# Performance work log

Hardware: AMD Instinct MI355X
Metric: run time of the kernel (lower is better)

The kernel has to match this reference:

```python
import jax, jax.numpy as jnp
from jax import lax
import numpy as np

T, B, D, H = 512, 256, 128, 256
SHIFT = 0.0


def setup_inputs() -> dict:
    key = jax.random.key(0)
    ks = jax.random.split(key, 11)
    s_in = 1.0 / np.sqrt(D + H)
    s_cl = 1.0 / np.sqrt(H)
    return {
        "inputs": jax.random.normal(ks[0], (T, B, D), dtype=jnp.float32),
        "Wf": jax.random.normal(ks[1], (H, D + H), dtype=jnp.float32) * s_in,
        "bf": jax.random.normal(ks[2], (H,), dtype=jnp.float32) * s_in,
        "Wi": jax.random.normal(ks[3], (H, D + H), dtype=jnp.float32) * s_in,
        "bi": jax.random.normal(ks[4], (H,), dtype=jnp.float32) * s_in,
        "Wg": jax.random.normal(ks[5], (H, D + H), dtype=jnp.float32) * s_in,
        "bg": jax.random.normal(ks[6], (H,), dtype=jnp.float32) * s_in,
        "Wo": jax.random.normal(ks[7], (H, D + H), dtype=jnp.float32) * s_in,
        "bo": jax.random.normal(ks[8], (H,), dtype=jnp.float32) * s_in,
        "Wc": jax.random.normal(ks[9], (1, H), dtype=jnp.float32) * s_cl,
        "bc": jax.random.normal(ks[10], (1,), dtype=jnp.float32) * s_cl,
    }


def reference(inputs, Wf, bf, Wi, bi, Wg, bg, Wo, bo, Wc, bc):
    # Fuse the four gate linears into one GEMM per step: [4H, D+H]
    W = jnp.concatenate([Wf, Wi, Wg, Wo], axis=0)
    b = jnp.concatenate([bf, bi, bg, bo], axis=0)
    h = W.shape[0] // 4
    batch = inputs.shape[1]

    def step(carry, x):
        hx, cx = carry
        combined = jnp.concatenate([x, hx], axis=1)      # [B, D+H]
        z = combined @ W.T + b                            # [B, 4H]
        f = jax.nn.sigmoid(z[:, 0 * h:1 * h])
        i = jax.nn.sigmoid(z[:, 1 * h:2 * h])
        g = jnp.tanh(z[:, 2 * h:3 * h])
        o = jax.nn.sigmoid(z[:, 3 * h:4 * h])
        cx = f * cx + i * g
        hx = o * jnp.tanh(cx)
        return (hx, cx), hx

    h0 = jnp.zeros((batch, h), dtype=inputs.dtype)
    c0 = jnp.zeros((batch, h), dtype=inputs.dtype)
    (hx, cx), hs = lax.scan(step, (h0, c0), inputs)       # hs: [T, B, H]

    logits = hs @ Wc.T + bc                               # [T, B, 1]
    probs = jax.nn.sigmoid(logits + SHIFT)
    return (jnp.concatenate([probs, 1.0 - probs], axis=-1), hx, cx)
```

## Files before the change

kernel.cpp:

```cpp
#include <hip/hip_runtime.h>
#include <hip/hip_bf16.h>
#include <hip/hip_cooperative_groups.h>

namespace cg = cooperative_groups;


#define T_STEPS 512
#define BATCH   256
#define DIN     128
#define HID     256
#define KDIM    384
#define LDK     392
#define GRIDN   256
#define NPOLL   96

typedef __attribute__((ext_vector_type(8))) short short8;
typedef __attribute__((ext_vector_type(4))) short short4v;
typedef __attribute__((ext_vector_type(4))) float f32x4;

__device__ unsigned boot_percxd[8];
__device__ unsigned boot_claimed[8];

__device__ __forceinline__ unsigned short f2bf(float f) {
    unsigned u = __float_as_uint(f);
    unsigned r = (u + 0x7FFFu + ((u >> 16) & 1u)) >> 16;
    return (unsigned short)r;
}
__device__ __forceinline__ float bf2f(unsigned short s) {
    return __uint_as_float(((unsigned)s) << 16);
}
__device__ __forceinline__ float sigmoid_f(float x) {
    return 1.f / (1.f + __expf(-x));
}
__device__ __forceinline__ float tanh_f(float x) {
    float e = __expf(2.f * x);
    return 1.f - 2.f / (e + 1.f);
}
__device__ __forceinline__ void poll_load_sc0(const unsigned int* p, uint4& a,
                                              uint4& b, uint4& c, uint4& d) {
    asm volatile(
        "global_load_dwordx4 %0, %4, off sc0\n\t"
        "global_load_dwordx4 %1, %4, off offset:16 sc0\n\t"
        "global_load_dwordx4 %2, %4, off offset:32 sc0\n\t"
        "global_load_dwordx4 %3, %4, off offset:48 sc0\n\t"
        "s_waitcnt vmcnt(0)"
        : "=&v"(a), "=&v"(b), "=&v"(c), "=&v"(d) : "v"(p) : "memory");
}
__device__ __forceinline__ void poll_load_sc1(const unsigned int* p, uint4& a,
                                              uint4& b, uint4& c, uint4& d) {
    asm volatile(
        "global_load_dwordx4 %0, %4, off sc1\n\t"
        "global_load_dwordx4 %1, %4, off offset:16 sc1\n\t"
        "global_load_dwordx4 %2, %4, off offset:32 sc1\n\t"
        "global_load_dwordx4 %3, %4, off offset:48 sc1\n\t"
        "s_waitcnt vmcnt(0)"
        : "=&v"(a), "=&v"(b), "=&v"(c), "=&v"(d) : "v"(p) : "memory");
}
__device__ __forceinline__ void store_plain_u32(unsigned int* p, unsigned int v) {
    asm volatile("global_store_dword %0, %1, off" :: "v"(p), "v"(v) : "memory");
}
__device__ __forceinline__ void store_sc1_u32(unsigned int* p, unsigned int v) {
    asm volatile("global_store_dword %0, %1, off sc1" :: "v"(p), "v"(v) : "memory");
}
__device__ __forceinline__ unsigned pack2bf(unsigned lo, unsigned hi) {
    return (hi & 0xFFFF0000u) | (lo >> 16);
}
__device__ __forceinline__ bool tags_ok(const uint4& a, const uint4& b,
                                        const uint4& c, const uint4& d,
                                        unsigned tag) {
    return ((a.x ^ tag) & 0xFFFFu) == 0 && ((a.y ^ tag) & 0xFFFFu) == 0 &&
           ((a.z ^ tag) & 0xFFFFu) == 0 && ((a.w ^ tag) & 0xFFFFu) == 0 &&
           ((b.x ^ tag) & 0xFFFFu) == 0 && ((b.y ^ tag) & 0xFFFFu) == 0 &&
           ((b.z ^ tag) & 0xFFFFu) == 0 && ((b.w ^ tag) & 0xFFFFu) == 0 &&
           ((c.x ^ tag) & 0xFFFFu) == 0 && ((c.y ^ tag) & 0xFFFFu) == 0 &&
           ((c.z ^ tag) & 0xFFFFu) == 0 && ((c.w ^ tag) & 0xFFFFu) == 0 &&
           ((d.x ^ tag) & 0xFFFFu) == 0 && ((d.y ^ tag) & 0xFFFFu) == 0 &&
           ((d.z ^ tag) & 0xFFFFu) == 0 && ((d.w ^ tag) & 0xFFFFu) == 0;
}

__global__ __launch_bounds__(256) void pack_w(
    const float* __restrict__ Wf, const float* __restrict__ Wi,
    const float* __restrict__ Wg, const float* __restrict__ Wo,
    unsigned short* __restrict__ Wp) {
    int idx = blockIdx.x * 256 + threadIdx.x;
    int n = idx / KDIM;
    int k = idx - n * KDIM;
    int g = n >> 8, j = n & 255;
    const float* s = (g == 0) ? Wf : (g == 1) ? Wi : (g == 2) ? Wg : Wo;
    Wp[idx] = f2bf(s[j * KDIM + k]);
}

__global__ __launch_bounds__(256) void pack_b(
    const float* __restrict__ bf, const float* __restrict__ bi,
    const float* __restrict__ bg, const float* __restrict__ bo,
    float* __restrict__ bp) {
    int n = blockIdx.x * 256 + threadIdx.x;
    int g = n >> 8, j = n & 255;
    const float* s = (g == 0) ? bf : (g == 1) ? bi : (g == 2) ? bg : bo;
    bp[n] = s[j];
}

__global__ __launch_bounds__(256) void init_k(unsigned int* __restrict__ hxp) {
    int tid = blockIdx.x * 256 + threadIdx.x;
    hxp[tid] = 0u;
    hxp[65536 + tid] = 0u;
    hxp[131072 + tid] = 0u;
    hxp[196608 + tid] = 0u;
    if (tid < 8) {
        boot_percxd[tid] = 0u;
        boot_claimed[tid] = 0u;
    }
}

__global__ __launch_bounds__(256, 1) void lstm_persist(
    const float* __restrict__ X,
    const unsigned short* __restrict__ W,
    const float* __restrict__ bias,
    unsigned int* __restrict__ hxp,
    unsigned short* __restrict__ hist,
    float* __restrict__ out) {
    __shared__ __align__(16) unsigned short W_s[64 * LDK];
    __shared__ __align__(16) unsigned short comb_s[16 * LDK];
    __shared__ __align__(16) float z_s[4 * 272];
    __shared__ int fastok_s;
    __shared__ int role_s;

    const int tid = threadIdx.x;

    if (tid == 0) {
        unsigned xcc = __builtin_amdgcn_s_getreg((31u << 11) | 20u) & 7u;
        unsigned slot = atomicAdd(&boot_percxd[xcc], 1u);
        int role = -1;
        if (slot < 32u) {
            role = (int)(xcc * 32u + slot);
            atomicOr(&boot_claimed[role >> 5], 1u << (role & 31));
        }
        role_s = role;
        fastok_s = 1;
    }
    __syncthreads();
    cg::this_grid().sync();
    if (role_s < 0) {
        if (tid == 0) {
            for (int r = 0; r < 256; ++r) {
                unsigned bit = 1u << (r & 31);
                if (!(atomicOr(&boot_claimed[r >> 5], bit) & bit)) {
                    role_s = r;
                    break;
                }
            }
        }
        __syncthreads();
    }
    const int role = role_s;
    const int bg = role >> 4, jg = role & 15;
    const int b0 = bg * 16, j0 = jg * 16;
    const int wave = tid >> 6, lane = tid & 63;
    const int l16 = lane & 15, quad = lane >> 4;
    const int bi = tid >> 4, jj = tid & 15;
    const int b = b0 + bi, j = j0 + jj;

#pragma unroll
    for (int c = 0; c < 12; ++c) {
        int q = c * 256 + tid;
        int row = q / 48, c8 = q - row * 48;
        int g = row >> 4, jr = row & 15;
        short8 v = *(const short8*)(W + ((g * 256 + j0 + jr) * KDIM + c8 * 8));
        *(short8*)(&W_s[row * LDK + c8 * 8]) = v;
    }
    const float bs0 = bias[0 * HID + j];
    const float bs1 = bias[1 * HID + j];
    const float bs2 = bias[2 * HID + j];
    const float bs3 = bias[3 * HID + j];

    float c_reg = 0.f;
    float h_final = 0.f;

    const unsigned short* arow = &comb_s[l16 * LDK + quad * 8];
    const unsigned short* brow = &W_s[(wave * 16 + l16) * LDK + quad * 8];
    const int hrow = tid >> 4, hc = tid & 15;
    const int xr0 = tid >> 5, xc4 = tid & 31, xr1 = (tid + 256) >> 5;

    const float* xb = X + b0 * DIN;
    float4 xv0 = *(const float4*)(xb + xr0 * DIN + xc4 * 4);
    float4 xv1 = *(const float4*)(xb + xr1 * DIN + xc4 * 4);

    __syncthreads();

    for (int k = 0; k < T_STEPS; ++k) {
        const unsigned tag = (unsigned)k;
        const unsigned int* fb =
            hxp + (k & 1) * 65536 + (b0 + hrow) * HID + hc * 16;
        const unsigned int* sb = fb + 131072;
        uint4 a, bq, cq, d;
        const int usefast = fastok_s;

        {
            short4v r;
            r.x = (short)f2bf(xv0.x); r.y = (short)f2bf(xv0.y);
            r.z = (short)f2bf(xv0.z); r.w = (short)f2bf(xv0.w);
            *(short4v*)(&comb_s[xr0 * LDK + xc4 * 4]) = r;
            r.x = (short)f2bf(xv1.x); r.y = (short)f2bf(xv1.y);
            r.z = (short)f2bf(xv1.z); r.w = (short)f2bf(xv1.w);
            *(short4v*)(&comb_s[xr1 * LDK + xc4 * 4]) = r;
        }

        if (usefast) {
            int tries = NPOLL;
            bool ok = false;
            for (;;) {
                poll_load_sc0(fb, a, bq, cq, d);
                if (tags_ok(a, bq, cq, d, tag)) { ok = true; break; }
                if (--tries == 0) break;
            }
            if (!ok) {
                fastok_s = 0;
                for (;;) {
                    poll_load_sc1(sb, a, bq, cq, d);
                    if (tags_ok(a, bq, cq, d, tag)) break;
                    __builtin_amdgcn_s_sleep(1);
                }
            }
        } else {
            for (;;) {
                poll_load_sc1(sb, a, bq, cq, d);
                if (tags_ok(a, bq, cq, d, tag)) break;
                __builtin_amdgcn_s_sleep(1);
            }
        }

        {
            uint4 p0, p1;
            p0.x = pack2bf(a.x, a.y);   p0.y = pack2bf(a.z, a.w);
            p0.z = pack2bf(bq.x, bq.y); p0.w = pack2bf(bq.z, bq.w);
            p1.x = pack2bf(cq.x, cq.y); p1.y = pack2bf(cq.z, cq.w);
            p1.z = pack2bf(d.x, d.y);   p1.w = pack2bf(d.z, d.w);
            *(uint4*)(&comb_s[hrow * LDK + DIN + hc * 16]) = p0;
            *(uint4*)(&comb_s[hrow * LDK + DIN + hc * 16 + 8]) = p1;
        }
        __syncthreads();

        f32x4 acc0 = {0.f, 0.f, 0.f, 0.f}, acc1 = {0.f, 0.f, 0.f, 0.f};
#pragma unroll
        for (int kt = 0; kt < 6; ++kt) {
            short8 a0 = *(const short8*)(arow + (2 * kt) * 32);
            short8 b0v = *(const short8*)(brow + (2 * kt) * 32);
            short8 a1 = *(const short8*)(arow + (2 * kt + 1) * 32);
            short8 b1v = *(const short8*)(brow + (2 * kt + 1) * 32);
            acc0 = __builtin_amdgcn_mfma_f32_16x16x32_bf16(a0, b0v, acc0, 0, 0, 0);
            acc1 = __builtin_amdgcn_mfma_f32_16x16x32_bf16(a1, b1v, acc1, 0, 0, 0);
        }
#pragma unroll
        for (int r = 0; r < 4; ++r)
            z_s[wave * 272 + (quad * 4 + r) * 17 + l16] = acc0[r] + acc1[r];
        __syncthreads();

        float zf = z_s[0 * 272 + bi * 17 + jj] + bs0;
        float zi = z_s[1 * 272 + bi * 17 + jj] + bs1;
        float zg = z_s[2 * 272 + bi * 17 + jj] + bs2;
        float zo = z_s[3 * 272 + bi * 17 + jj] + bs3;
        float fg = sigmoid_f(zf);
        float ig = sigmoid_f(zi);
        float gg = tanh_f(zg);
        float og = sigmoid_f(zo);
        c_reg = fg * c_reg + ig * gg;
        float hval = og * tanh_f(c_reg);
        unsigned short hb = f2bf(hval);
        unsigned int hword = ((unsigned)hb << 16) | (unsigned)(k + 1);
        unsigned int* fdst = hxp + ((k + 1) & 1) * 65536 + b * HID + j;
        store_plain_u32(fdst, hword);
        store_sc1_u32(fdst + 131072, hword);
        hist[(size_t)k * BATCH * HID + b * HID + j] = hb;
        if (k + 1 < T_STEPS) {
            const float* xn = X + (size_t)(k + 1) * BATCH * DIN + b0 * DIN;
            xv0 = *(const float4*)(xn + xr0 * DIN + xc4 * 4);
            xv1 = *(const float4*)(xn + xr1 * DIN + xc4 * 4);
        } else {
            h_final = hval;
        }
    }

    out[T_STEPS * BATCH * 2 + b * HID + j] = h_final;
    out[T_STEPS * BATCH * 2 + BATCH * HID + b * HID + j] = c_reg;
}

__global__ __launch_bounds__(256) void probs_k(
    const unsigned short* __restrict__ hist, const float* __restrict__ Wc,
    const float* __restrict__ bc, float* __restrict__ out) {
    const int wave = threadIdx.x >> 6, lane = threadIdx.x & 63;
    const size_t row = (size_t)blockIdx.x * 4 + wave;
    const unsigned short* h = hist + row * HID;
    short4v hv = *(const short4v*)(h + lane * 4);
    const float4 wv = *(const float4*)(Wc + lane * 4);
    float p = bf2f((unsigned short)hv.x) * wv.x + bf2f((unsigned short)hv.y) * wv.y +
              bf2f((unsigned short)hv.z) * wv.z + bf2f((unsigned short)hv.w) * wv.w;
#pragma unroll
    for (int off = 32; off >= 1; off >>= 1) p += __shfl_down(p, off);
    if (lane == 0) {
        float prob = 1.f / (1.f + __expf(-(p + bc[0])));
        out[row * 2]     = prob;
        out[row * 2 + 1] = 1.f - prob;
    }
}

extern "C" void kernel_launch(void* const* d_in, const int* in_sizes, int n_in,
                              void* d_out, int out_size, void* d_ws, size_t ws_size,
                              hipStream_t stream) {
    const float* X  = (const float*)d_in[0];
    const float* Wf = (const float*)d_in[1];
    const float* bfp= (const float*)d_in[2];
    const float* Wi = (const float*)d_in[3];
    const float* bip= (const float*)d_in[4];
    const float* Wg = (const float*)d_in[5];
    const float* bgp= (const float*)d_in[6];
    const float* Wo = (const float*)d_in[7];
    const float* bop= (const float*)d_in[8];
    const float* Wc = (const float*)d_in[9];
    const float* bc = (const float*)d_in[10];
    float* out = (float*)d_out;

    char* ws = (char*)d_ws;
    unsigned short* Wpack = (unsigned short*)(ws);
    float* bias = (float*)(ws + 786432);
    unsigned int* hxp = (unsigned int*)(ws + 790528);
    unsigned short* hist = (unsigned short*)(ws + 1839104);

    pack_w<<<1536, 256, 0, stream>>>(Wf, Wi, Wg, Wo, Wpack);
    pack_b<<<4, 256, 0, stream>>>(bfp, bip, bgp, bop, bias);
    init_k<<<256, 256, 0, stream>>>(hxp);

    void* kargs[6] = {(void*)&X, (void*)&Wpack, (void*)&bias,
                      (void*)&hxp, (void*)&hist, (void*)&out};
    (void)hipLaunchCooperativeKernel((const void*)lstm_persist, dim3(GRIDN),
                                     dim3(256), kargs, 0, stream);

    probs_k<<<32768, 256, 0, stream>>>(hist, Wc, bc, out);
}
```

Before: 1.203 ms.

## Add helper wave for slow-path publishing and history stores in persistent LSTM

Adds a fifth wavefront per block that picks up freshly computed h words from LDS and issues the sc1 slow-path global stores and the bf16 history writes. The compute waves no longer stall on those stores. The change also double-buffers the X prefetch two steps ahead and moves the next step's X conversion into the post-GEMM phase. The trade-off is a larger block, extra LDS polling and a padding array that forces one block per CU, plus the risk that the slow-path publication now lags by a wave handoff.

```diff
diff --git a/kernel.cpp b/kernel.cpp
--- a/kernel.cpp
+++ b/kernel.cpp
@@ -12,6 +12,8 @@
 #define KDIM    384
 #define LDK     392
 #define GRIDN   256
+#define BLOCKT  320
+#define NCOMP   256
 #define NPOLL   96
 
 typedef __attribute__((ext_vector_type(8))) short short8;
@@ -112,7 +114,7 @@
     }
 }
 
-__global__ __launch_bounds__(256, 1) void lstm_persist(
+__global__ __launch_bounds__(BLOCKT, 1) void lstm_persist(
     const float* __restrict__ X,
     const unsigned short* __restrict__ W,
     const float* __restrict__ bias,
@@ -122,6 +124,8 @@
     __shared__ __align__(16) unsigned short W_s[64 * LDK];
     __shared__ __align__(16) unsigned short comb_s[16 * LDK];
     __shared__ __align__(16) float z_s[4 * 272];
+    __shared__ __align__(16) unsigned hw_lds[NCOMP];
+    __shared__ char pad_s[32768];
     __shared__ int fastok_s;
     __shared__ int role_s;
 
@@ -153,6 +157,8 @@
         __syncthreads();
     }
     const int role = role_s;
+    if (role == -12345) pad_s[0] = 1;
+
     const int bg = role >> 4, jg = role & 15;
     const int b0 = bg * 16, j0 = jg * 16;
     const int wave = tid >> 6, lane = tid & 63;
@@ -160,18 +166,24 @@
     const int bi = tid >> 4, jj = tid & 15;
     const int b = b0 + bi, j = j0 + jj;
 
+    if (tid < NCOMP) {
 #pragma unroll
-    for (int c = 0; c < 12; ++c) {
-        int q = c * 256 + tid;
-        int row = q / 48, c8 = q - row * 48;
-        int g = row >> 4, jr = row & 15;
-        short8 v = *(const short8*)(W + ((g * 256 + j0 + jr) * KDIM + c8 * 8));
-        *(short8*)(&W_s[row * LDK + c8 * 8]) = v;
-    }
-    const float bs0 = bias[0 * HID + j];
-    const float bs1 = bias[1 * HID + j];
-    const float bs2 = bias[2 * HID + j];
-    const float bs3 = bias[3 * HID + j];
+        for (int c = 0; c < 12; ++c) {
+            int q = c * 256 + tid;
+            int row = q / 48, c8 = q - row * 48;
+            int g = row >> 4, jr = row & 15;
+            short8 v = *(const short8*)(W + ((g * 256 + j0 + jr) * KDIM + c8 * 8));
+            *(short8*)(&W_s[row * LDK + c8 * 8]) = v;
+        }
+        hw_lds[tid] = 0u;
+    }
+    float bs0 = 0.f, bs1 = 0.f, bs2 = 0.f, bs3 = 0.f;
+    if (tid < NCOMP) {
+        bs0 = bias[0 * HID + j];
+        bs1 = bias[1 * HID + j];
+        bs2 = bias[2 * HID + j];
+        bs3 = bias[3 * HID + j];
+    }
 
     float c_reg = 0.f;
     float h_final = 0.f;
@@ -181,55 +193,73 @@
     const int hrow = tid >> 4, hc = tid & 15;
     const int xr0 = tid >> 5, xc4 = tid & 31, xr1 = (tid + 256) >> 5;
 
-    const float* xb = X + b0 * DIN;
-    float4 xv0 = *(const float4*)(xb + xr0 * DIN + xc4 * 4);
-    float4 xv1 = *(const float4*)(xb + xr1 * DIN + xc4 * 4);
-
+    const int sv = tid - NCOMP;
+    const int t4 = sv * 4;
+    const int bs_b = b0 + (t4 >> 4), bs_j = j0 + (t4 & 15);
+
+    float4 xA0, xA1, xB0, xB1;
+    if (tid < NCOMP) {
+        const float* x0b = X + b0 * DIN;
+        float4 t0 = *(const float4*)(x0b + xr0 * DIN + xc4 * 4);
+        float4 t1 = *(const float4*)(x0b + xr1 * DIN + xc4 * 4);
+        short4v r;
+        r.x = (short)f2bf(t0.x); r.y = (short)f2bf(t0.y);
+        r.z = (short)f2bf(t0.z); r.w = (short)f2bf(t0.w);
+        *(short4v*)(&comb_s[xr0 * LDK + xc4 * 4]) = r;
+        r.x = (short)f2bf(t1.x); r.y = (short)f2bf(t1.y);
+        r.z = (short)f2bf(t1.z); r.w = (short)f2bf(t1.w);
+        *(short4v*)(&comb_s[xr1 * LDK + xc4 * 4]) = r;
+        const float* x1b = X + (size_t)1 * BATCH * DIN + b0 * DIN;
+        xB0 = *(const float4*)(x1b + xr0 * DIN + xc4 * 4);
+        xB1 = *(const float4*)(x1b + xr1 * DIN + xc4 * 4);
+    }
     __syncthreads();
 
     for (int k = 0; k < T_STEPS; ++k) {
-        const unsigned tag = (unsigned)k;
-        const unsigned int* fb =
-            hxp + (k & 1) * 65536 + (b0 + hrow) * HID + hc * 16;
-        const unsigned int* sb = fb + 131072;
-        uint4 a, bq, cq, d;
-        const int usefast = fastok_s;
-
-        {
-            short4v r;
-            r.x = (short)f2bf(xv0.x); r.y = (short)f2bf(xv0.y);
-            r.z = (short)f2bf(xv0.z); r.w = (short)f2bf(xv0.w);
-            *(short4v*)(&comb_s[xr0 * LDK + xc4 * 4]) = r;
-            r.x = (short)f2bf(xv1.x); r.y = (short)f2bf(xv1.y);
-            r.z = (short)f2bf(xv1.z); r.w = (short)f2bf(xv1.w);
-            *(short4v*)(&comb_s[xr1 * LDK + xc4 * 4]) = r;
-        }
-
-        if (usefast) {
-            int tries = NPOLL;
-            bool ok = false;
-            for (;;) {
-                poll_load_sc0(fb, a, bq, cq, d);
-                if (tags_ok(a, bq, cq, d, tag)) { ok = true; break; }
-                if (--tries == 0) break;
-            }
-            if (!ok) {
-                fastok_s = 0;
+        if (tid < NCOMP) {
+            const unsigned tag = (unsigned)k;
+            const unsigned int* fb =
+                hxp + (k & 1) * 65536 + (b0 + hrow) * HID + hc * 16;
+            const unsigned int* sb = fb + 131072;
+            uint4 a, bq, cq, d;
+            const int usefast = fastok_s;
+
+            if (usefast) {
+                int tries = NPOLL;
+                bool ok = false;
+                for (;;) {
+                    poll_load_sc0(fb, a, bq, cq, d);
+                    if (tags_ok(a, bq, cq, d, tag)) { ok = true; break; }
+                    if (--tries == 0) break;
+                }
+                if (!ok) {
+                    fastok_s = 0;
+                    for (;;) {
+                        poll_load_sc1(sb, a, bq, cq, d);
+                        if (tags_ok(a, bq, cq, d, tag)) break;
+                        __builtin_amdgcn_s_sleep(1);
+                    }
+                }
+            } else {
                 for (;;) {
                     poll_load_sc1(sb, a, bq, cq, d);
                     if (tags_ok(a, bq, cq, d, tag)) break;
                     __builtin_amdgcn_s_sleep(1);
                 }
             }
-        } else {
-            for (;;) {
-                poll_load_sc1(sb, a, bq, cq, d);
-                if (tags_ok(a, bq, cq, d, tag)) break;
-                __builtin_amdgcn_s_sleep(1);
-            }
-        }
-
-        {
+
+            if (k + 2 < T_STEPS) {
+                const float* xn = X + (size_t)(k + 2) * BATCH * DIN + b0 * DIN;
+                if (k & 1) {
+                    xB0 = *(const float4*)(xn + xr0 * DIN + xc4 * 4);
+                    xB1 = *(const float4*)(xn + xr1 * DIN + xc4 * 4);
+                } else {
+                    xA0 = *(const float4*)(xn + xr0 * DIN + xc4 * 4);
+                    xA1 = *(const float4*)(xn + xr1 * DIN + xc4 * 4);
+                }
+            }
+            __builtin_amdgcn_sched_barrier(0);
+
             uint4 p0, p1;
             p0.x = pack2bf(a.x, a.y);   p0.y = pack2bf(a.z, a.w);
             p0.z = pack2bf(bq.x, bq.y); p0.w = pack2bf(bq.z, bq.w);
@@ -237,51 +267,104 @@
             p1.z = pack2bf(d.x, d.y);   p1.w = pack2bf(d.z, d.w);
             *(uint4*)(&comb_s[hrow * LDK + DIN + hc * 16]) = p0;
             *(uint4*)(&comb_s[hrow * LDK + DIN + hc * 16 + 8]) = p1;
+        } else if (k > 0) {
+            volatile unsigned* hw = hw_lds;
+            unsigned w0, w1, w2, w3;
+            const unsigned tag = (unsigned)k;
+            for (;;) {
+                w0 = hw[t4]; w1 = hw[t4 + 1]; w2 = hw[t4 + 2]; w3 = hw[t4 + 3];
+                if (((w0 ^ tag) & 0xFFFFu) == 0 && ((w1 ^ tag) & 0xFFFFu) == 0 &&
+                    ((w2 ^ tag) & 0xFFFFu) == 0 && ((w3 ^ tag) & 0xFFFFu) == 0)
+                    break;
+            }
+            unsigned int* sd =
+                hxp + 131072 + (k & 1) * 65536 + bs_b * HID + bs_j;
+            store_sc1_u32(sd + 0, w0);
+            store_sc1_u32(sd + 1, w1);
+            store_sc1_u32(sd + 2, w2);
+            store_sc1_u32(sd + 3, w3);
+            uint2 hp;
+            hp.x = pack2bf(w0, w1);
+            hp.y = pack2bf(w2, w3);
+            *(uint2*)(&hist[(size_t)(k - 1) * BATCH * HID +
+                            (size_t)bs_b * HID + bs_j]) = hp;
+            asm volatile("s_waitcnt vmcnt(16)" ::: "memory");
         }
         __syncthreads();
 
-        f32x4 acc0 = {0.f, 0.f, 0.f, 0.f}, acc1 = {0.f, 0.f, 0.f, 0.f};
+        if (tid < NCOMP) {
+            f32x4 acc0 = {0.f, 0.f, 0.f, 0.f}, acc1 = {0.f, 0.f, 0.f, 0.f};
 #pragma unroll
-        for (int kt = 0; kt < 6; ++kt) {
-            short8 a0 = *(const short8*)(arow + (2 * kt) * 32);
-            short8 b0v = *(const short8*)(brow + (2 * kt) * 32);
-            short8 a1 = *(const short8*)(arow + (2 * kt + 1) * 32);
-            short8 b1v = *(const short8*)(brow + (2 * kt + 1) * 32);
-            acc0 = __builtin_amdgcn_mfma_f32_16x16x32_bf16(a0, b0v, acc0, 0, 0, 0);
-            acc1 = __builtin_amdgcn_mfma_f32_16x16x32_bf16(a1, b1v, acc1, 0, 0, 0);
-        }
+            for (int kt = 0; kt < 6; ++kt) {
+                short8 a0 = *(const short8*)(arow + (2 * kt) * 32);
+                short8 b0v = *(const short8*)(brow + (2 * kt) * 32);
+                short8 a1 = *(const short8*)(arow + (2 * kt + 1) * 32);
+                short8 b1v = *(const short8*)(brow + (2 * kt + 1) * 32);
+                acc0 = __builtin_amdgcn_mfma_f32_16x16x32_bf16(a0, b0v, acc0, 0, 0, 0);
+                acc1 = __builtin_amdgcn_mfma_f32_16x16x32_bf16(a1, b1v, acc1, 0, 0, 0);
+            }
 #pragma unroll
-        for (int r = 0; r < 4; ++r)
-            z_s[wave * 272 + (quad * 4 + r) * 17 + l16] = acc0[r] + acc1[r];
+            for (int r = 0; r < 4; ++r)
+                z_s[wave * 272 + (quad * 4 + r) * 17 + l16] = acc0[r] + acc1[r];
+        }
         __syncthreads();
 
-        float zf = z_s[0 * 272 + bi * 17 + jj] + bs0;
-        float zi = z_s[1 * 272 + bi * 17 + jj] + bs1;
-        float zg = z_s[2 * 272 + bi * 17 + jj] + bs2;
-        float zo = z_s[3 * 272 + bi * 17 + jj] + bs3;
-        float fg = sigmoid_f(zf);
-        float ig = sigmoid_f(zi);
-        float gg = tanh_f(zg);
-        float og = sigmoid_f(zo);
-        c_reg = fg * c_reg + ig * gg;
-        float hval = og * tanh_f(c_reg);
-        unsigned short hb = f2bf(hval);
-        unsigned int hword = ((unsigned)hb << 16) | (unsigned)(k + 1);
-        unsigned int* fdst = hxp + ((k + 1) & 1) * 65536 + b * HID + j;
-        store_plain_u32(fdst, hword);
-        store_sc1_u32(fdst + 131072, hword);
-        hist[(size_t)k * BATCH * HID + b * HID + j] = hb;
-        if (k + 1 < T_STEPS) {
-            const float* xn = X + (size_t)(k + 1) * BATCH * DIN + b0 * DIN;
-            xv0 = *(const float4*)(xn + xr0 * DIN + xc4 * 4);
-            xv1 = *(const float4*)(xn + xr1 * DIN + xc4 * 4);
-        } else {
-            h_final = hval;
-        }
-    }
-
-    out[T_STEPS * BATCH * 2 + b * HID + j] = h_final;
-    out[T_STEPS * BATCH * 2 + BATCH * HID + b * HID + j] = c_reg;
+        if (tid < NCOMP) {
+            if (k + 1 < T_STEPS) {
+                float4 s0 = ((k + 1) & 1) ? xB0 : xA0;
+                float4 s1 = ((k + 1) & 1) ? xB1 : xA1;
+                short4v r;
+                r.x = (short)f2bf(s0.x); r.y = (short)f2bf(s0.y);
+                r.z = (short)f2bf(s0.z); r.w = (short)f2bf(s0.w);
+                *(short4v*)(&comb_s[xr0 * LDK + xc4 * 4]) = r;
+                r.x = (short)f2bf(s1.x); r.y = (short)f2bf(s1.y);
+                r.z = (short)f2bf(s1.z); r.w = (short)f2bf(s1.w);
+                *(short4v*)(&comb_s[xr1 * LDK + xc4 * 4]) = r;
+            }
+            float zf = z_s[0 * 272 + bi * 17 + jj] + bs0;
+            float zi = z_s[1 * 272 + bi * 17 + jj] + bs1;
+            float zg = z_s[2 * 272 + bi * 17 + jj] + bs2;
+            float zo = z_s[3 * 272 + bi * 17 + jj] + bs3;
+            float fg = sigmoid_f(zf);
+            float ig = sigmoid_f(zi);
+            float gg = tanh_f(zg);
+            float og = sigmoid_f(zo);
+            c_reg = fg * c_reg + ig * gg;
+            float hval = og * tanh_f(c_reg);
+            unsigned short hb = f2bf(hval);
+            unsigned int hword = ((unsigned)hb << 16) | (unsigned)(k + 1);
+            unsigned int* fdst = hxp + ((k + 1) & 1) * 65536 + b * HID + j;
+            store_plain_u32(fdst, hword);
+            ((volatile unsigned*)hw_lds)[tid] = hword;
+            if (k + 1 == T_STEPS) h_final = hval;
+        }
+    }
+
+    if (tid >= NCOMP) {
+        volatile unsigned* hw = hw_lds;
+        unsigned w0, w1, w2, w3;
+        const unsigned tag = (unsigned)T_STEPS;
+        for (;;) {
+            w0 = hw[t4]; w1 = hw[t4 + 1]; w2 = hw[t4 + 2]; w3 = hw[t4 + 3];
+            if (((w0 ^ tag) & 0xFFFFu) == 0 && ((w1 ^ tag) & 0xFFFFu) == 0 &&
+                ((w2 ^ tag) & 0xFFFFu) == 0 && ((w3 ^ tag) & 0xFFFFu) == 0)
+                break;
+        }
+        unsigned int* sd =
+            hxp + 131072 + (T_STEPS & 1) * 65536 + bs_b * HID + bs_j;
+        store_sc1_u32(sd + 0, w0);
+        store_sc1_u32(sd + 1, w1);
+        store_sc1_u32(sd + 2, w2);
+        store_sc1_u32(sd + 3, w3);
+        uint2 hp;
+        hp.x = pack2bf(w0, w1);
+        hp.y = pack2bf(w2, w3);
+        *(uint2*)(&hist[(size_t)(T_STEPS - 1) * BATCH * HID +
+                        (size_t)bs_b * HID + bs_j]) = hp;
+    } else {
+        out[T_STEPS * BATCH * 2 + b * HID + j] = h_final;
+        out[T_STEPS * BATCH * 2 + BATCH * HID + b * HID + j] = c_reg;
+    }
 }
 
 __global__ __launch_bounds__(256) void probs_k(
@@ -332,7 +415,7 @@
     void* kargs[6] = {(void*)&X, (void*)&Wpack, (void*)&bias,
                       (void*)&hxp, (void*)&hist, (void*)&out};
     (void)hipLaunchCooperativeKernel((const void*)lstm_persist, dim3(GRIDN),
-                                     dim3(256), kargs, 0, stream);
+                                     dim3(BLOCKT), kargs, 0, stream);
 
     probs_k<<<32768, 256, 0, stream>>>(hist, Wc, bc, out);
 }
```

New measurement: 4.613 ms. 283% more time.
